# Kernel tuning notes

Hardware: AMD Instinct MI355X
Metric: run time of the kernel (lower is better)

The kernel has to match this reference:

```python
import jax, jax.numpy as jnp
import numpy as np

N_NODES = 20000


def _segment_softmax(alpha, dst, num_nodes):
    # numerically-stable softmax over edges grouped by destination node
    m = jax.ops.segment_max(alpha, dst, num_segments=num_nodes)
    m = jnp.where(jnp.isfinite(m), m, 0.0)
    a = jnp.exp(alpha - m[dst])
    denom = jax.ops.segment_sum(a, dst, num_segments=num_nodes)
    return a / denom[dst]


def mgcn_conv(x, src, dst, edge_type, basis, att, weight, root, bias, num_nodes):
    # x: [N, in], basis: [B, in, out], att: [R, B], weight: [R, out=in]
    x_i = x[dst]                                   # [E, in] target feats
    x_j = x[src]                                   # [E, in] source feats
    # per-edge attention logit: sum_d x_i[d] * w_r[d] * x_j[d]
    alpha = jnp.sum(x_i * weight[edge_type] * x_j, axis=1)   # [E]
    alpha = _segment_softmax(alpha, dst, num_nodes)          # [E]
    # basis-decomposed per-edge transform: x_j @ (att_r . basis)
    t = jnp.einsum('ei,bio->ebo', x_j, basis)                # [E, B, out]
    msg = jnp.einsum('ebo,eb->eo', t, att[edge_type])        # [E, out]
    msg = msg * alpha[:, None]
    out = jax.ops.segment_sum(msg, dst, num_segments=num_nodes)  # [N, out]
    return out + x @ root + bias


def setup_inputs() -> dict:
    key = jax.random.key(0)
    ks = jax.random.split(key, 16)
    E, D, R, B, N = 32768, 128, 474, 64, N_NODES
    s = 0.05
    return {
        'entity': jnp.arange(N, dtype=jnp.int64) if jax.config.jax_enable_x64 else jnp.arange(N, dtype=jnp.int32),
        'edge_index': jax.random.randint(ks[0], (2, E), 0, N, dtype=jnp.int32),
        'edge_type': jax.random.randint(ks[1], (E,), 0, R, dtype=jnp.int32),
        'emb_table': jax.random.normal(ks[2], (N, D), dtype=jnp.float32),
        'basis1': jax.random.normal(ks[3], (B, D, D), dtype=jnp.float32) * s,
        'att1': jax.random.normal(ks[4], (R, B), dtype=jnp.float32) * s,
        'weight1': jax.random.normal(ks[5], (R, D), dtype=jnp.float32) * s,
        'root1': jax.random.normal(ks[6], (D, D), dtype=jnp.float32) * s,
        'bias1': jnp.zeros((D,), dtype=jnp.float32),
        'basis2': jax.random.normal(ks[7], (B, D, D), dtype=jnp.float32) * s,
        'att2': jax.random.normal(ks[8], (R, B), dtype=jnp.float32) * s,
        'weight2': jax.random.normal(ks[9], (R, D), dtype=jnp.float32) * s,
        'root2': jax.random.normal(ks[10], (D, D), dtype=jnp.float32) * s,
        'bias2': jnp.zeros((D,), dtype=jnp.float32),
    }


def reference(entity, edge_index, edge_type, emb_table,
              basis1, att1, weight1, root1, bias1,
              basis2, att2, weight2, root2, bias2):
    src, dst = edge_index[0], edge_index[1]   # PyG: (source j, target i)
    x = emb_table[entity]                     # embedding lookup
    h = jax.nn.relu(mgcn_conv(x, src, dst, edge_type, basis1, att1,
                              weight1, root1, bias1, N_NODES))
    # dropout is identity at inference
    out = mgcn_conv(h, src, dst, edge_type, basis2, att2,
                    weight2, root2, bias2, N_NODES)
    return out
```

## Files before the change

### kernel.cpp

```cpp
#include <hip/hip_runtime.h>
#include <hip/hip_bf16.h>

#define N_NODES 20000
#define N_EDGES 32768
#define DIM 128
#define N_REL 474
#define N_BASIS 64
#define TILE_E 64
#define WSTRIDE 264
#define WMIX_BLKS 128
#define TR_BLKS 2
#define GATHER_BASE (WMIX_BLKS + TR_BLKS)
#define FIN_BLKS ((N_NODES + 63) / 64)
#define LELIST 1024

typedef __bf16 bf16x8 __attribute__((ext_vector_type(8)));
typedef float f32x4 __attribute__((ext_vector_type(4)));

__device__ __forceinline__ unsigned short f2b(float f) {
    unsigned u = __float_as_uint(f);
    unsigned r = (u + 0x7FFFu + ((u >> 16) & 1u)) >> 16;
    return (unsigned short)r;
}
__device__ __forceinline__ float b2f(unsigned short s) {
    return __uint_as_float(((unsigned)s) << 16);
}
__device__ __forceinline__ __bf16 u2b(unsigned short u) {
    union { unsigned short u; __bf16 b; } c; c.u = u; return c.b;
}
__device__ __forceinline__ float dot2bf(unsigned a, unsigned b, float wx, float wy) {
    return b2f((unsigned short)(a & 0xFFFFu)) * wx * b2f((unsigned short)(b & 0xFFFFu))
         + b2f((unsigned short)(a >> 16)) * wy * b2f((unsigned short)(b >> 16));
}

__global__ __launch_bounds__(256) void prep_kernel(const float4* __restrict__ emb,
                                                   const int* __restrict__ entity,
                                                   ushort4* __restrict__ xb4,
                                                   float4* __restrict__ zreg, int zcount4,
                                                   const float* __restrict__ att1,
                                                   const float* __restrict__ basis1,
                                                   unsigned short* __restrict__ W1,
                                                   const float* __restrict__ att2,
                                                   const float* __restrict__ basis2,
                                                   unsigned short* __restrict__ W2,
                                                   const float* __restrict__ root1,
                                                   unsigned short* __restrict__ rootT1,
                                                   const float* __restrict__ root2,
                                                   unsigned short* __restrict__ rootT2) {
    __shared__ __align__(16) unsigned short bt[64 * WSTRIDE];
    int t = threadIdx.x;
    if (blockIdx.x < WMIX_BLKS) {
        int wi = blockIdx.x;
        const float* att   = (wi >= 64) ? att2 : att1;
        const float* basis = (wi >= 64) ? basis2 : basis1;
        unsigned short* W  = (wi >= 64) ? W2 : W1;
        int io0 = (wi & 63) * 256;
#pragma unroll
        for (int p = 0; p < 16; p++) {
            int c = t + 256 * p;
            int k = c >> 6, of = c & 63;
            float4 v = *(const float4*)(basis + (size_t)k * (DIM * DIM) + io0 + of * 4);
            ushort4 s;
            s.x = f2b(v.x); s.y = f2b(v.y); s.z = f2b(v.z); s.w = f2b(v.w);
            int ofx = of ^ (((k >> 3) & 7) << 2);
            *(ushort4*)&bt[k * WSTRIDE + ofx * 4] = s;
        }
        __syncthreads();

        int w = t >> 6, l = t & 63, n = l & 15, q = l >> 4;
        bf16x8 bfr[2][4];
#pragma unroll
        for (int kb = 0; kb < 2; kb++) {
            int kbase = kb * 32 + q * 8;
            int sx = ((kb * 4 + q) & 7) << 4;
#pragma unroll
            for (int c = 0; c < 4; c++) {
                int ob = (w * 64 + c * 16 + n) ^ sx;
#pragma unroll
                for (int j = 0; j < 8; j++) bfr[kb][c][j] = u2b(bt[(kbase + j) * WSTRIDE + ob]);
            }
        }
#pragma unroll 1
        for (int rg = 0; rg < 8; rg++) {
            int r0 = rg * 64;
            f32x4 acc[4][4] = {};
#pragma unroll
            for (int kb = 0; kb < 2; kb++) {
                int kbase = kb * 32 + q * 8;
                bf16x8 a[4];
#pragma unroll
                for (int rt = 0; rt < 4; rt++) {
                    int rm = min(r0 + rt * 16 + n, N_REL - 1);
                    const float4* ap = (const float4*)(att + (size_t)rm * N_BASIS + kbase);
                    float4 u0 = ap[0], u1 = ap[1];
                    a[rt][0] = (__bf16)u0.x; a[rt][1] = (__bf16)u0.y;
                    a[rt][2] = (__bf16)u0.z; a[rt][3] = (__bf16)u0.w;
                    a[rt][4] = (__bf16)u1.x; a[rt][5] = (__bf16)u1.y;
                    a[rt][6] = (__bf16)u1.z; a[rt][7] = (__bf16)u1.w;
                }
#pragma unroll
                for (int c = 0; c < 4; c++) {
#pragma unroll
                    for (int rt = 0; rt < 4; rt++)
                        acc[rt][c] = __builtin_amdgcn_mfma_f32_16x16x32_bf16(a[rt], bfr[kb][c], acc[rt][c], 0, 0, 0);
                }
            }
#pragma unroll
            for (int rt = 0; rt < 4; rt++) {
#pragma unroll
                for (int c = 0; c < 4; c++) {
                    int col = io0 + w * 64 + c * 16 + n;
#pragma unroll
                    for (int g = 0; g < 4; g++) {
                        int r = r0 + rt * 16 + q * 4 + g;
                        if (r < N_REL) W[(size_t)r * (DIM * DIM) + col] = f2b(acc[rt][c][g]);
                    }
                }
            }
        }
    } else if (blockIdx.x < GATHER_BASE) {
        int wi2 = blockIdx.x - WMIX_BLKS;
        const float* rm = wi2 ? root2 : root1;
        unsigned short* rt_ = wi2 ? rootT2 : rootT1;
        unsigned short* sb16 = bt;
#pragma unroll
        for (int p = 0; p < 16; p++) {
            int idx = t + 256 * p;
            int k = idx >> 5, o4 = idx & 31;
            float4 v = ((const float4*)rm)[idx];
            ushort4 s;
            s.x = f2b(v.x); s.y = f2b(v.y); s.z = f2b(v.z); s.w = f2b(v.w);
            *(ushort4*)&sb16[k * 132 + o4 * 4] = s;
        }
        __syncthreads();
        int o = t >> 1, kh = (t & 1) * 64;
#pragma unroll
        for (int i = 0; i < 16; i++) {
            int k0 = kh + i * 4;
            ushort4 s;
            s.x = sb16[(k0 + 0) * 132 + o];
            s.y = sb16[(k0 + 1) * 132 + o];
            s.z = sb16[(k0 + 2) * 132 + o];
            s.w = sb16[(k0 + 3) * 132 + o];
            *(ushort4*)&rt_[o * DIM + k0] = s;
        }
    } else {
        int pb = blockIdx.x - GATHER_BASE;
        int gtid = pb * 256 + t;
        int gsz = 1024 * 256;
        int total4 = N_NODES * DIM / 4;
        for (int i = gtid; i < total4; i += gsz) {
            int n = i >> 5, rem = i & 31;
            float4 v = emb[(size_t)entity[n] * 32 + rem];
            ushort4 s;
            s.x = f2b(v.x); s.y = f2b(v.y); s.z = f2b(v.z); s.w = f2b(v.w);
            xb4[i] = s;
        }
        float4 z = make_float4(0.f, 0.f, 0.f, 0.f);
        for (int i = gtid; i < zcount4; i += gsz) zreg[i] = z;
    }
}

__global__ __launch_bounds__(256) void msg_kernel(const unsigned short* __restrict__ xb,
                                                  const unsigned short* __restrict__ W,
                                                  const float* __restrict__ wlog,
                                                  const int* __restrict__ src,
                                                  const int* __restrict__ dst,
                                                  const int* __restrict__ etype,
                                                  float* __restrict__ den,
                                                  float* __restrict__ accm) {
    int r = blockIdx.x;
    const unsigned short* Wr = W + (size_t)r * (DIM * DIM);

    __shared__ __align__(16) unsigned short wt[128 * 136];
    __shared__ __align__(16) unsigned short xjf[8192];
    __shared__ __align__(16) float wf[DIM];
    __shared__ float scf[TILE_E];
    __shared__ int sdd[TILE_E];
    __shared__ int ssrc[TILE_E];
    __shared__ int elist[LELIST];
    __shared__ int lcnt;

    int t = threadIdx.x;
    if (t == 0) lcnt = 0;
#pragma unroll
    for (int p = 0; p < 8; p++) {
        int c = t + 256 * p;
        int k = c >> 4, oct = c & 15;
        int4 v = *(const int4*)(Wr + k * DIM + oct * 8);
        int oct2 = oct ^ (((k >> 3) & 7) << 1);
        *(int4*)&wt[k * 136 + oct2 * 8] = v;
    }
    if (t < 32) ((float4*)wf)[t] = ((const float4*)(wlog + (size_t)r * DIM))[t];
    __syncthreads();

    int lane = t & 63;
    for (int it = 0; it < N_EDGES / 1024; it++) {
        int idx = it * 256 + t;
        int4 ev = ((const int4*)etype)[idx];
#pragma unroll
        for (int j = 0; j < 4; j++) {
            int etj = (j == 0) ? ev.x : (j == 1) ? ev.y : (j == 2) ? ev.z : ev.w;
            bool m = (etj == r);
            unsigned long long bal = __ballot(m);
            int tot = __popcll(bal);
            if (tot) {
                int base = 0;
                if (lane == 0) base = atomicAdd(&lcnt, tot);
                base = __shfl(base, 0, 64);
                if (m) {
                    int pre = __popcll(bal & ((1ull << lane) - 1ull));
                    int p_ = base + pre;
                    if (p_ < LELIST) elist[p_] = idx * 4 + j;
                }
            }
        }
    }
    __syncthreads();
    int cnt = min(lcnt, LELIST);
    if (cnt == 0) return;

    int w = t >> 6, l = t & 63, n = l & 15, q = l >> 4;
    int el4 = t >> 2, l4 = t & 3;

    for (int t0 = 0; t0 < cnt; t0 += TILE_E) {
        int nE = min(TILE_E, cnt - t0);
        if (t < TILE_E) {
            if (t < nE) {
                int e = elist[t0 + t];
                ssrc[t] = src[e];
                sdd[t]  = dst[e];
            } else { ssrc[t] = 0; sdd[t] = 0; }
        }
        __syncthreads();

        {
            int s_ = ssrc[el4], d_ = sdd[el4];
            const int4* xj = (const int4*)(xb + (size_t)s_ * DIM) + l4 * 4;
            const int4* xi = (const int4*)(xb + (size_t)d_ * DIM) + l4 * 4;
            const float4* wv = (const float4*)&wf[l4 * 32];
            float v = 0.f;
#pragma unroll
            for (int u = 0; u < 4; u++) {
                int4 a = xj[u]; int4 b = xi[u];
                float4 w0 = wv[u * 2], w1 = wv[u * 2 + 1];
                v += dot2bf((unsigned)a.x, (unsigned)b.x, w0.x, w0.y)
                   + dot2bf((unsigned)a.y, (unsigned)b.y, w0.z, w0.w)
                   + dot2bf((unsigned)a.z, (unsigned)b.z, w1.x, w1.y)
                   + dot2bf((unsigned)a.w, (unsigned)b.w, w1.z, w1.w);
            }
            v += __shfl_xor(v, 1, 64);
            v += __shfl_xor(v, 2, 64);
            if (l4 == 0) {
                if (el4 < nE) {
                    float a = expf(v);
                    scf[el4] = a;
                    atomicAdd(&den[d_], a);
                } else scf[el4] = 0.f;
            }
        }

#pragma unroll
        for (int p = 0; p < 4; p++) {
            int c = t + 256 * p;
            int g = c >> 6;
            int rt = g >> 2, kb = g & 3;
            int q2 = (c >> 4) & 3, m = c & 15;
            int e = rt * 16 + m;
            int oct = kb * 4 + q2;
            int4 v = make_int4(0, 0, 0, 0);
            if (e < nE) v = *(const int4*)(xb + (size_t)ssrc[e] * DIM + oct * 8);
            *(int4*)&xjf[c * 8] = v;
        }
        __syncthreads();

        f32x4 acc[2][4] = {};
#pragma unroll
        for (int kb = 0; kb < 4; kb++) {
            bf16x8 a[4];
#pragma unroll
            for (int rt = 0; rt < 4; rt++) a[rt] = *(const bf16x8*)&xjf[((rt * 4 + kb) * 64 + l) * 8];
            int kbase = kb * 32 + q * 8;
            int sx = ((kb * 4 + q) & 7) << 4;
#pragma unroll
            for (int c = 0; c < 2; c++) {
                int ob = ((w * 2 + c) * 16 + n) ^ sx;
                bf16x8 b;
#pragma unroll
                for (int j = 0; j < 8; j++) b[j] = u2b(wt[(kbase + j) * 136 + ob]);
#pragma unroll
                for (int rt = 0; rt < 4; rt++)
                    acc[c][rt] = __builtin_amdgcn_mfma_f32_16x16x32_bf16(a[rt], b, acc[c][rt], 0, 0, 0);
            }
        }
#pragma unroll
        for (int c = 0; c < 2; c++) {
            int col = (w * 2 + c) * 16 + n;
#pragma unroll
            for (int rt = 0; rt < 4; rt++) {
#pragma unroll
                for (int rg = 0; rg < 4; rg++) {
                    int e = rt * 16 + q * 4 + rg;
                    if (e < nE)
                        atomicAdd(&accm[(size_t)sdd[e] * DIM + col], scf[e] * acc[c][rt][rg]);
                }
            }
        }
        __syncthreads();
    }
}

__global__ __launch_bounds__(256) void fin_kernel(const unsigned short* __restrict__ xb,
                                                  const unsigned short* __restrict__ rootT,
                                                  const float* __restrict__ bias,
                                                  const float* __restrict__ accm,
                                                  const float* __restrict__ den,
                                                  float* __restrict__ outf,
                                                  unsigned short* __restrict__ outb) {
    __shared__ __align__(16) unsigned short xrf[8192];
    int t = threadIdx.x;
    int n0 = blockIdx.x * 64;
#pragma unroll
    for (int p = 0; p < 4; p++) {
        int c = t + 256 * p;
        int g = c >> 6;
        int rt = g >> 2, kb = g & 3;
        int q = (c >> 4) & 3, m = c & 15;
        int row = n0 + rt * 16 + m;
        int oct = kb * 4 + q;
        int4 v = make_int4(0, 0, 0, 0);
        if (row < N_NODES) v = *(const int4*)(xb + (size_t)row * DIM + oct * 8);
        *(int4*)&xrf[c * 8] = v;
    }
    __syncthreads();

    int w_ = t >> 6, l = t & 63, n = l & 15, q = l >> 4;
    f32x4 acc[2][4] = {};
#pragma unroll
    for (int kb = 0; kb < 4; kb++) {
        bf16x8 a[4];
#pragma unroll
        for (int rt = 0; rt < 4; rt++) a[rt] = *(const bf16x8*)&xrf[((rt * 4 + kb) * 64 + l) * 8];
        int kbase = kb * 32 + q * 8;
#pragma unroll
        for (int c = 0; c < 2; c++) {
            int col = (w_ * 2 + c) * 16 + n;
            bf16x8 b = *(const bf16x8*)(rootT + (size_t)col * DIM + kbase);
#pragma unroll
            for (int rt = 0; rt < 4; rt++)
                acc[c][rt] = __builtin_amdgcn_mfma_f32_16x16x32_bf16(a[rt], b, acc[c][rt], 0, 0, 0);
        }
    }
#pragma unroll
    for (int c = 0; c < 2; c++) {
        int col = (w_ * 2 + c) * 16 + n;
        float bo = bias[col];
#pragma unroll
        for (int rt = 0; rt < 4; rt++) {
#pragma unroll
            for (int rg = 0; rg < 4; rg++) {
                int row = n0 + rt * 16 + q * 4 + rg;
                if (row < N_NODES) {
                    float dv = den[row];
                    float mv = accm[(size_t)row * DIM + col];
                    float val = acc[c][rt][rg] + bo + (dv > 0.f ? mv / dv : 0.f);
                    if (outb) outb[(size_t)row * DIM + col] = f2b(fmaxf(val, 0.f));
                    else      outf[(size_t)row * DIM + col] = val;
                }
            }
        }
    }
}

extern "C" void kernel_launch(void* const* d_in, const int* in_sizes, int n_in,
                              void* d_out, int out_size, void* d_ws, size_t ws_size,
                              hipStream_t stream) {
    const int N = N_NODES, E = N_EDGES, R = N_REL;

    const int* entity = (const int*)d_in[0];
    const int* eidx   = (const int*)d_in[1];
    const int* src    = eidx;
    const int* dst    = eidx + E;
    const int* etype  = (const int*)d_in[2];
    const float* emb  = (const float*)d_in[3];
    const float* basis1 = (const float*)d_in[4];
    const float* att1   = (const float*)d_in[5];
    const float* w1     = (const float*)d_in[6];
    const float* root1  = (const float*)d_in[7];
    const float* bias1  = (const float*)d_in[8];
    const float* basis2 = (const float*)d_in[9];
    const float* att2   = (const float*)d_in[10];
    const float* w2     = (const float*)d_in[11];
    const float* root2  = (const float*)d_in[12];
    const float* bias2  = (const float*)d_in[13];
    float* out = (float*)d_out;

    size_t off = 0;
    auto alloc = [&](size_t bytes) -> void* {
        void* p = (char*)d_ws + off;
        off += (bytes + 255) & ~(size_t)255;
        return p;
    };
    unsigned short* W1 = (unsigned short*)alloc((size_t)R * DIM * DIM * 2);
    unsigned short* W2 = (unsigned short*)alloc((size_t)R * DIM * DIM * 2);
    unsigned short* xb = (unsigned short*)alloc((size_t)N * DIM * 2);
    unsigned short* hb = (unsigned short*)alloc((size_t)N * DIM * 2);
    float* zreg   = (float*)alloc(((size_t)2 * N + (size_t)2 * N * DIM) * 4);
    float* den1   = zreg;
    float* den2   = zreg + N;
    float* accm1  = zreg + 2 * N;
    float* accm2  = zreg + 2 * N + (size_t)N * DIM;
    unsigned short* rootT1 = (unsigned short*)alloc((size_t)DIM * DIM * 2);
    unsigned short* rootT2 = (unsigned short*)alloc((size_t)DIM * DIM * 2);

    int zcount4 = (2 * N + 2 * N * DIM) / 4;

    prep_kernel<<<GATHER_BASE + 1024, 256, 0, stream>>>(
        (const float4*)emb, entity, (ushort4*)xb, (float4*)zreg, zcount4,
        att1, basis1, W1, att2, basis2, W2, root1, rootT1, root2, rootT2);

    msg_kernel<<<N_REL, 256, 0, stream>>>(xb, W1, w1, src, dst, etype, den1, accm1);
    fin_kernel<<<FIN_BLKS, 256, 0, stream>>>(xb, rootT1, bias1, accm1, den1, nullptr, hb);

    msg_kernel<<<N_REL, 256, 0, stream>>>(hb, W2, w2, src, dst, etype, den2, accm2);
    fin_kernel<<<FIN_BLKS, 256, 0, stream>>>(hb, rootT2, bias2, accm2, den2, out, nullptr);
}
```

Baseline: 227.9 us.

## Split relation blocks in half, fold root GEMM into prep/msg, add merge kernel

Each relation now gets two message blocks, each scanning half of the edge types, which doubles the grid to spread work across more CUs. The root (x @ root) GEMM moves out of the finalize kernel: for layer 1 it runs inside prep blocks, and for layer 2 as extra blocks in the message kernel. A lightweight vectorized merge kernel then combines root, message and denominator. The W mix output is staged through LDS so global stores are 16-byte vectorized. In exchange it writes and reads extra fp32 racc buffers and adds redundant W tile loads per relation half.

New measurement: 215.3 us. 5.5% less time.

```diff
diff --git a/kernel.cpp b/kernel.cpp
--- a/kernel.cpp
+++ b/kernel.cpp
@@ -8,11 +8,17 @@
 #define N_BASIS 64
 #define TILE_E 64
 #define WSTRIDE 264
+#define LELIST 1024
+
 #define WMIX_BLKS 128
-#define TR_BLKS 2
-#define GATHER_BASE (WMIX_BLKS + TR_BLKS)
-#define FIN_BLKS ((N_NODES + 63) / 64)
-#define LELIST 1024
+#define ROOTT_BLK 1
+#define RG1_BASE (WMIX_BLKS + ROOTT_BLK)
+#define RG1_BLKS ((N_NODES + 63) / 64)
+#define GATHER_BASE (RG1_BASE + RG1_BLKS)
+#define PREP_GRID 1024
+
+#define MSG_REL_BLKS (2 * N_REL)
+#define MERGE_GRID 1024
 
 typedef __bf16 bf16x8 __attribute__((ext_vector_type(8)));
 typedef float f32x4 __attribute__((ext_vector_type(4)));
@@ -27,6 +33,14 @@
 }
 __device__ __forceinline__ __bf16 u2b(unsigned short u) {
     union { unsigned short u; __bf16 b; } c; c.u = u; return c.b;
+}
+__device__ __forceinline__ int4 pack8(float4 a0, float4 a1) {
+    int4 v;
+    v.x = (int)((unsigned)f2b(a0.x) | ((unsigned)f2b(a0.y) << 16));
+    v.y = (int)((unsigned)f2b(a0.z) | ((unsigned)f2b(a0.w) << 16));
+    v.z = (int)((unsigned)f2b(a1.x) | ((unsigned)f2b(a1.y) << 16));
+    v.w = (int)((unsigned)f2b(a1.z) | ((unsigned)f2b(a1.w) << 16));
+    return v;
 }
 __device__ __forceinline__ float dot2bf(unsigned a, unsigned b, float wx, float wy) {
     return b2f((unsigned short)(a & 0xFFFFu)) * wx * b2f((unsigned short)(b & 0xFFFFu))
@@ -44,7 +58,7 @@
                                                    const float* __restrict__ basis2,
                                                    unsigned short* __restrict__ W2,
                                                    const float* __restrict__ root1,
-                                                   unsigned short* __restrict__ rootT1,
+                                                   float* __restrict__ racc1,
                                                    const float* __restrict__ root2,
                                                    unsigned short* __restrict__ rootT2) {
     __shared__ __align__(16) unsigned short bt[64 * WSTRIDE];
@@ -80,6 +94,9 @@
                 for (int j = 0; j < 8; j++) bfr[kb][c][j] = u2b(bt[(kbase + j) * WSTRIDE + ob]);
             }
         }
+        __syncthreads();
+
+        int srow = t >> 2, sseg = t & 3;
 #pragma unroll 1
         for (int rg = 0; rg < 8; rg++) {
             int r0 = rg * 64;
@@ -109,25 +126,32 @@
             for (int rt = 0; rt < 4; rt++) {
 #pragma unroll
                 for (int c = 0; c < 4; c++) {
-                    int col = io0 + w * 64 + c * 16 + n;
-#pragma unroll
-                    for (int g = 0; g < 4; g++) {
-                        int r = r0 + rt * 16 + q * 4 + g;
-                        if (r < N_REL) W[(size_t)r * (DIM * DIM) + col] = f2b(acc[rt][c][g]);
-                    }
-                }
-            }
-        }
-    } else if (blockIdx.x < GATHER_BASE) {
-        int wi2 = blockIdx.x - WMIX_BLKS;
-        const float* rm = wi2 ? root2 : root1;
-        unsigned short* rt_ = wi2 ? rootT2 : rootT1;
+#pragma unroll
+                    for (int g = 0; g < 4; g++)
+                        bt[(rt * 16 + q * 4 + g) * WSTRIDE + w * 64 + c * 16 + n] = f2b(acc[rt][c][g]);
+                }
+            }
+            __syncthreads();
+            int rr = r0 + srow;
+            if (rr < N_REL) {
+                const int4* sp = (const int4*)&bt[srow * WSTRIDE];
+                unsigned short* wp = W + (size_t)rr * (DIM * DIM) + io0;
+#pragma unroll
+                for (int ii = 0; ii < 8; ii++) {
+                    int i = (ii + sseg * 2) & 7;
+                    int4 v = sp[sseg * 8 + i];
+                    *(int4*)(wp + sseg * 64 + i * 8) = v;
+                }
+            }
+            __syncthreads();
+        }
+    } else if (blockIdx.x < RG1_BASE) {
         unsigned short* sb16 = bt;
 #pragma unroll
         for (int p = 0; p < 16; p++) {
             int idx = t + 256 * p;
             int k = idx >> 5, o4 = idx & 31;
-            float4 v = ((const float4*)rm)[idx];
+            float4 v = ((const float4*)root2)[idx];
             ushort4 s;
             s.x = f2b(v.x); s.y = f2b(v.y); s.z = f2b(v.z); s.w = f2b(v.w);
             *(ushort4*)&sb16[k * 132 + o4 * 4] = s;
@@ -142,12 +166,64 @@
             s.y = sb16[(k0 + 1) * 132 + o];
             s.z = sb16[(k0 + 2) * 132 + o];
             s.w = sb16[(k0 + 3) * 132 + o];
-            *(ushort4*)&rt_[o * DIM + k0] = s;
+            *(ushort4*)&rootT2[o * DIM + k0] = s;
+        }
+    } else if (blockIdx.x < GATHER_BASE) {
+        int n0 = (blockIdx.x - RG1_BASE) * 64;
+        unsigned short* xrf = bt;
+#pragma unroll
+        for (int p = 0; p < 4; p++) {
+            int c = t + 256 * p;
+            int g = c >> 6;
+            int rt = g >> 2, kb = g & 3;
+            int q2 = (c >> 4) & 3, m = c & 15;
+            int row = n0 + rt * 16 + m;
+            int oct = kb * 4 + q2;
+            int4 v = make_int4(0, 0, 0, 0);
+            if (row < N_NODES) {
+                const float4* sp = emb + (size_t)entity[row] * 32 + oct * 2;
+                v = pack8(sp[0], sp[1]);
+            }
+            *(int4*)&xrf[c * 8] = v;
+        }
+        __syncthreads();
+
+        int w_ = t >> 6, l = t & 63, n = l & 15, q = l >> 4;
+        f32x4 acc[2][4] = {};
+#pragma unroll
+        for (int kb = 0; kb < 4; kb++) {
+            bf16x8 a[4];
+#pragma unroll
+            for (int rt = 0; rt < 4; rt++) a[rt] = *(const bf16x8*)&xrf[((rt * 4 + kb) * 64 + l) * 8];
+            int kbase = kb * 32 + q * 8;
+#pragma unroll
+            for (int c = 0; c < 2; c++) {
+                int col = (w_ * 2 + c) * 16 + n;
+                bf16x8 b;
+#pragma unroll
+                for (int j = 0; j < 8; j++) b[j] = (__bf16)root1[(kbase + j) * DIM + col];
+#pragma unroll
+                for (int rt = 0; rt < 4; rt++)
+                    acc[c][rt] = __builtin_amdgcn_mfma_f32_16x16x32_bf16(a[rt], b, acc[c][rt], 0, 0, 0);
+            }
+        }
+#pragma unroll
+        for (int c = 0; c < 2; c++) {
+            int col = (w_ * 2 + c) * 16 + n;
+#pragma unroll
+            for (int rt = 0; rt < 4; rt++) {
+#pragma unroll
+                for (int rg = 0; rg < 4; rg++) {
+                    int row = n0 + rt * 16 + q * 4 + rg;
+                    if (row < N_NODES)
+                        racc1[(size_t)row * DIM + col] = acc[c][rt][rg];
+                }
+            }
         }
     } else {
         int pb = blockIdx.x - GATHER_BASE;
         int gtid = pb * 256 + t;
-        int gsz = 1024 * 256;
+        int gsz = (PREP_GRID - GATHER_BASE) * 256;
         int total4 = N_NODES * DIM / 4;
         for (int i = gtid; i < total4; i += gsz) {
             int n = i >> 5, rem = i & 31;
@@ -168,10 +244,9 @@
                                                   const int* __restrict__ dst,
                                                   const int* __restrict__ etype,
                                                   float* __restrict__ den,
-                                                  float* __restrict__ accm) {
-    int r = blockIdx.x;
-    const unsigned short* Wr = W + (size_t)r * (DIM * DIM);
-
+                                                  float* __restrict__ accm,
+                                                  const unsigned short* __restrict__ rootT,
+                                                  float* __restrict__ racc) {
     __shared__ __align__(16) unsigned short wt[128 * 136];
     __shared__ __align__(16) unsigned short xjf[8192];
     __shared__ __align__(16) float wf[DIM];
@@ -182,192 +257,213 @@
     __shared__ int lcnt;
 
     int t = threadIdx.x;
-    if (t == 0) lcnt = 0;
-#pragma unroll
-    for (int p = 0; p < 8; p++) {
-        int c = t + 256 * p;
-        int k = c >> 4, oct = c & 15;
-        int4 v = *(const int4*)(Wr + k * DIM + oct * 8);
-        int oct2 = oct ^ (((k >> 3) & 7) << 1);
-        *(int4*)&wt[k * 136 + oct2 * 8] = v;
-    }
-    if (t < 32) ((float4*)wf)[t] = ((const float4*)(wlog + (size_t)r * DIM))[t];
-    __syncthreads();
-
-    int lane = t & 63;
-    for (int it = 0; it < N_EDGES / 1024; it++) {
-        int idx = it * 256 + t;
-        int4 ev = ((const int4*)etype)[idx];
-#pragma unroll
-        for (int j = 0; j < 4; j++) {
-            int etj = (j == 0) ? ev.x : (j == 1) ? ev.y : (j == 2) ? ev.z : ev.w;
-            bool m = (etj == r);
-            unsigned long long bal = __ballot(m);
-            int tot = __popcll(bal);
-            if (tot) {
-                int base = 0;
-                if (lane == 0) base = atomicAdd(&lcnt, tot);
-                base = __shfl(base, 0, 64);
-                if (m) {
-                    int pre = __popcll(bal & ((1ull << lane) - 1ull));
-                    int p_ = base + pre;
-                    if (p_ < LELIST) elist[p_] = idx * 4 + j;
-                }
-            }
-        }
-    }
-    __syncthreads();
-    int cnt = min(lcnt, LELIST);
-    if (cnt == 0) return;
-
-    int w = t >> 6, l = t & 63, n = l & 15, q = l >> 4;
-    int el4 = t >> 2, l4 = t & 3;
-
-    for (int t0 = 0; t0 < cnt; t0 += TILE_E) {
-        int nE = min(TILE_E, cnt - t0);
-        if (t < TILE_E) {
-            if (t < nE) {
-                int e = elist[t0 + t];
-                ssrc[t] = src[e];
-                sdd[t]  = dst[e];
-            } else { ssrc[t] = 0; sdd[t] = 0; }
-        }
-        __syncthreads();
-
-        {
-            int s_ = ssrc[el4], d_ = sdd[el4];
-            const int4* xj = (const int4*)(xb + (size_t)s_ * DIM) + l4 * 4;
-            const int4* xi = (const int4*)(xb + (size_t)d_ * DIM) + l4 * 4;
-            const float4* wv = (const float4*)&wf[l4 * 32];
-            float v = 0.f;
-#pragma unroll
-            for (int u = 0; u < 4; u++) {
-                int4 a = xj[u]; int4 b = xi[u];
-                float4 w0 = wv[u * 2], w1 = wv[u * 2 + 1];
-                v += dot2bf((unsigned)a.x, (unsigned)b.x, w0.x, w0.y)
-                   + dot2bf((unsigned)a.y, (unsigned)b.y, w0.z, w0.w)
-                   + dot2bf((unsigned)a.z, (unsigned)b.z, w1.x, w1.y)
-                   + dot2bf((unsigned)a.w, (unsigned)b.w, w1.z, w1.w);
-            }
-            v += __shfl_xor(v, 1, 64);
-            v += __shfl_xor(v, 2, 64);
-            if (l4 == 0) {
-                if (el4 < nE) {
-                    float a = expf(v);
-                    scf[el4] = a;
-                    atomicAdd(&den[d_], a);
-                } else scf[el4] = 0.f;
-            }
-        }
-
+    if ((int)blockIdx.x < MSG_REL_BLKS) {
+        int r = blockIdx.x >> 1, half = blockIdx.x & 1;
+        const unsigned short* Wr = W + (size_t)r * (DIM * DIM);
+        if (t == 0) lcnt = 0;
+#pragma unroll
+        for (int p = 0; p < 8; p++) {
+            int c = t + 256 * p;
+            int k = c >> 4, oct = c & 15;
+            int4 v = *(const int4*)(Wr + k * DIM + oct * 8);
+            int oct2 = oct ^ (((k >> 3) & 7) << 1);
+            *(int4*)&wt[k * 136 + oct2 * 8] = v;
+        }
+        if (t < 32) ((float4*)wf)[t] = ((const float4*)(wlog + (size_t)r * DIM))[t];
+        __syncthreads();
+
+        int lane = t & 63;
+        for (int it = half * 16; it < half * 16 + 16; it++) {
+            int idx = it * 256 + t;
+            int4 ev = ((const int4*)etype)[idx];
+#pragma unroll
+            for (int j = 0; j < 4; j++) {
+                int etj = (j == 0) ? ev.x : (j == 1) ? ev.y : (j == 2) ? ev.z : ev.w;
+                bool m = (etj == r);
+                unsigned long long bal = __ballot(m);
+                int tot = __popcll(bal);
+                if (tot) {
+                    int base = 0;
+                    if (lane == 0) base = atomicAdd(&lcnt, tot);
+                    base = __shfl(base, 0, 64);
+                    if (m) {
+                        int pre = __popcll(bal & ((1ull << lane) - 1ull));
+                        int p_ = base + pre;
+                        if (p_ < LELIST) elist[p_] = idx * 4 + j;
+                    }
+                }
+            }
+        }
+        __syncthreads();
+        int cnt = min(lcnt, LELIST);
+        if (cnt == 0) return;
+
+        int w = t >> 6, l = t & 63, n = l & 15, q = l >> 4;
+        int el4 = t >> 2, l4 = t & 3;
+
+        for (int t0 = 0; t0 < cnt; t0 += TILE_E) {
+            int nE = min(TILE_E, cnt - t0);
+            if (t < TILE_E) {
+                if (t < nE) {
+                    int e = elist[t0 + t];
+                    ssrc[t] = src[e];
+                    sdd[t]  = dst[e];
+                } else { ssrc[t] = 0; sdd[t] = 0; }
+            }
+            __syncthreads();
+
+            {
+                int s_ = ssrc[el4], d_ = sdd[el4];
+                const int4* xj = (const int4*)(xb + (size_t)s_ * DIM) + l4 * 4;
+                const int4* xi = (const int4*)(xb + (size_t)d_ * DIM) + l4 * 4;
+                const float4* wv = (const float4*)&wf[l4 * 32];
+                float v = 0.f;
+#pragma unroll
+                for (int u = 0; u < 4; u++) {
+                    int4 a = xj[u]; int4 bb = xi[u];
+                    float4 w0 = wv[u * 2], w1 = wv[u * 2 + 1];
+                    v += dot2bf((unsigned)a.x, (unsigned)bb.x, w0.x, w0.y)
+                       + dot2bf((unsigned)a.y, (unsigned)bb.y, w0.z, w0.w)
+                       + dot2bf((unsigned)a.z, (unsigned)bb.z, w1.x, w1.y)
+                       + dot2bf((unsigned)a.w, (unsigned)bb.w, w1.z, w1.w);
+                }
+                v += __shfl_xor(v, 1, 64);
+                v += __shfl_xor(v, 2, 64);
+                if (l4 == 0) {
+                    if (el4 < nE) {
+                        float a = expf(v);
+                        scf[el4] = a;
+                        atomicAdd(&den[d_], a);
+                    } else scf[el4] = 0.f;
+                }
+            }
+
+#pragma unroll
+            for (int p = 0; p < 4; p++) {
+                int c = t + 256 * p;
+                int g = c >> 6;
+                int rt = g >> 2, kb = g & 3;
+                int q2 = (c >> 4) & 3, m = c & 15;
+                int e = rt * 16 + m;
+                int oct = kb * 4 + q2;
+                int4 v = make_int4(0, 0, 0, 0);
+                if (e < nE) v = *(const int4*)(xb + (size_t)ssrc[e] * DIM + oct * 8);
+                *(int4*)&xjf[c * 8] = v;
+            }
+            __syncthreads();
+
+            f32x4 acc[2][4] = {};
+#pragma unroll
+            for (int kb = 0; kb < 4; kb++) {
+                bf16x8 a[4];
+#pragma unroll
+                for (int rt = 0; rt < 4; rt++) a[rt] = *(const bf16x8*)&xjf[((rt * 4 + kb) * 64 + l) * 8];
+                int kbase = kb * 32 + q * 8;
+                int sx = ((kb * 4 + q) & 7) << 4;
+#pragma unroll
+                for (int c = 0; c < 2; c++) {
+                    int ob = ((w * 2 + c) * 16 + n) ^ sx;
+                    bf16x8 bb;
+#pragma unroll
+                    for (int j = 0; j < 8; j++) bb[j] = u2b(wt[(kbase + j) * 136 + ob]);
+#pragma unroll
+                    for (int rt = 0; rt < 4; rt++)
+                        acc[c][rt] = __builtin_amdgcn_mfma_f32_16x16x32_bf16(a[rt], bb, acc[c][rt], 0, 0, 0);
+                }
+            }
+#pragma unroll
+            for (int c = 0; c < 2; c++) {
+                int col = (w * 2 + c) * 16 + n;
+#pragma unroll
+                for (int rt = 0; rt < 4; rt++) {
+#pragma unroll
+                    for (int rg = 0; rg < 4; rg++) {
+                        int e = rt * 16 + q * 4 + rg;
+                        if (e < nE)
+                            atomicAdd(&accm[(size_t)sdd[e] * DIM + col], scf[e] * acc[c][rt][rg]);
+                    }
+                }
+            }
+            __syncthreads();
+        }
+    } else {
+        int n0 = ((int)blockIdx.x - MSG_REL_BLKS) * 64;
+        unsigned short* xrf = wt;
 #pragma unroll
         for (int p = 0; p < 4; p++) {
             int c = t + 256 * p;
             int g = c >> 6;
             int rt = g >> 2, kb = g & 3;
             int q2 = (c >> 4) & 3, m = c & 15;
-            int e = rt * 16 + m;
+            int row = n0 + rt * 16 + m;
             int oct = kb * 4 + q2;
             int4 v = make_int4(0, 0, 0, 0);
-            if (e < nE) v = *(const int4*)(xb + (size_t)ssrc[e] * DIM + oct * 8);
-            *(int4*)&xjf[c * 8] = v;
-        }
-        __syncthreads();
-
+            if (row < N_NODES) v = *(const int4*)(xb + (size_t)row * DIM + oct * 8);
+            *(int4*)&xrf[c * 8] = v;
+        }
+        __syncthreads();
+
+        int w_ = t >> 6, l = t & 63, n = l & 15, q = l >> 4;
         f32x4 acc[2][4] = {};
 #pragma unroll
         for (int kb = 0; kb < 4; kb++) {
             bf16x8 a[4];
 #pragma unroll
-            for (int rt = 0; rt < 4; rt++) a[rt] = *(const bf16x8*)&xjf[((rt * 4 + kb) * 64 + l) * 8];
+            for (int rt = 0; rt < 4; rt++) a[rt] = *(const bf16x8*)&xrf[((rt * 4 + kb) * 64 + l) * 8];
             int kbase = kb * 32 + q * 8;
-            int sx = ((kb * 4 + q) & 7) << 4;
 #pragma unroll
             for (int c = 0; c < 2; c++) {
-                int ob = ((w * 2 + c) * 16 + n) ^ sx;
-                bf16x8 b;
-#pragma unroll
-                for (int j = 0; j < 8; j++) b[j] = u2b(wt[(kbase + j) * 136 + ob]);
+                int col = (w_ * 2 + c) * 16 + n;
+                bf16x8 bb = *(const bf16x8*)(rootT + (size_t)col * DIM + kbase);
 #pragma unroll
                 for (int rt = 0; rt < 4; rt++)
-                    acc[c][rt] = __builtin_amdgcn_mfma_f32_16x16x32_bf16(a[rt], b, acc[c][rt], 0, 0, 0);
-            }
-        }
-#pragma unroll
-        for (int c = 0; c < 2; c++) {
-            int col = (w * 2 + c) * 16 + n;
-#pragma unroll
-            for (int rt = 0; rt < 4; rt++) {
-#pragma unroll
-                for (int rg = 0; rg < 4; rg++) {
-                    int e = rt * 16 + q * 4 + rg;
-                    if (e < nE)
-                        atomicAdd(&accm[(size_t)sdd[e] * DIM + col], scf[e] * acc[c][rt][rg]);
-                }
-            }
-        }
-        __syncthreads();
-    }
-}
-
-__global__ __launch_bounds__(256) void fin_kernel(const unsigned short* __restrict__ xb,
-                                                  const unsigned short* __restrict__ rootT,
-                                                  const float* __restrict__ bias,
-                                                  const float* __restrict__ accm,
-                                                  const float* __restrict__ den,
-                                                  float* __restrict__ outf,
-                                                  unsigned short* __restrict__ outb) {
-    __shared__ __align__(16) unsigned short xrf[8192];
-    int t = threadIdx.x;
-    int n0 = blockIdx.x * 64;
-#pragma unroll
-    for (int p = 0; p < 4; p++) {
-        int c = t + 256 * p;
-        int g = c >> 6;
-        int rt = g >> 2, kb = g & 3;
-        int q = (c >> 4) & 3, m = c & 15;
-        int row = n0 + rt * 16 + m;
-        int oct = kb * 4 + q;
-        int4 v = make_int4(0, 0, 0, 0);
-        if (row < N_NODES) v = *(const int4*)(xb + (size_t)row * DIM + oct * 8);
-        *(int4*)&xrf[c * 8] = v;
-    }
-    __syncthreads();
-
-    int w_ = t >> 6, l = t & 63, n = l & 15, q = l >> 4;
-    f32x4 acc[2][4] = {};
-#pragma unroll
-    for (int kb = 0; kb < 4; kb++) {
-        bf16x8 a[4];
-#pragma unroll
-        for (int rt = 0; rt < 4; rt++) a[rt] = *(const bf16x8*)&xrf[((rt * 4 + kb) * 64 + l) * 8];
-        int kbase = kb * 32 + q * 8;
+                    acc[c][rt] = __builtin_amdgcn_mfma_f32_16x16x32_bf16(a[rt], bb, acc[c][rt], 0, 0, 0);
+            }
+        }
 #pragma unroll
         for (int c = 0; c < 2; c++) {
             int col = (w_ * 2 + c) * 16 + n;
-            bf16x8 b = *(const bf16x8*)(rootT + (size_t)col * DIM + kbase);
-#pragma unroll
-            for (int rt = 0; rt < 4; rt++)
-                acc[c][rt] = __builtin_amdgcn_mfma_f32_16x16x32_bf16(a[rt], b, acc[c][rt], 0, 0, 0);
+#pragma unroll
+            for (int rt = 0; rt < 4; rt++) {
+#pragma unroll
+                for (int rg = 0; rg < 4; rg++) {
+                    int row = n0 + rt * 16 + q * 4 + rg;
+                    if (row < N_NODES)
+                        racc[(size_t)row * DIM + col] = acc[c][rt][rg];
+                }
+            }
         }
     }
-#pragma unroll
-    for (int c = 0; c < 2; c++) {
-        int col = (w_ * 2 + c) * 16 + n;
-        float bo = bias[col];
-#pragma unroll
-        for (int rt = 0; rt < 4; rt++) {
-#pragma unroll
-            for (int rg = 0; rg < 4; rg++) {
-                int row = n0 + rt * 16 + q * 4 + rg;
-                if (row < N_NODES) {
-                    float dv = den[row];
-                    float mv = accm[(size_t)row * DIM + col];
-                    float val = acc[c][rt][rg] + bo + (dv > 0.f ? mv / dv : 0.f);
-                    if (outb) outb[(size_t)row * DIM + col] = f2b(fmaxf(val, 0.f));
-                    else      outf[(size_t)row * DIM + col] = val;
-                }
-            }
+}
+
+__global__ __launch_bounds__(256) void merge_kernel(const float4* __restrict__ racc,
+                                                    const float4* __restrict__ accm,
+                                                    const float* __restrict__ den,
+                                                    const float* __restrict__ bias,
+                                                    float4* __restrict__ outf,
+                                                    ushort4* __restrict__ outb) {
+    int gtid = blockIdx.x * 256 + threadIdx.x;
+    const int tot4 = N_NODES * (DIM / 4);
+    for (int i = gtid; i < tot4; i += (int)gridDim.x * 256) {
+        int row = i >> 5;
+        int c0 = (i & 31) * 4;
+        float4 rv = racc[i];
+        float4 mv = accm[i];
+        float4 bo = *(const float4*)&bias[c0];
+        float dv = den[row];
+        float inv = dv > 0.f ? 1.0f / dv : 0.f;
+        float4 v;
+        v.x = rv.x + bo.x + mv.x * inv;
+        v.y = rv.y + bo.y + mv.y * inv;
+        v.z = rv.z + bo.z + mv.z * inv;
+        v.w = rv.w + bo.w + mv.w * inv;
+        if (outb) {
+            ushort4 s;
+            s.x = f2b(fmaxf(v.x, 0.f)); s.y = f2b(fmaxf(v.y, 0.f));
+            s.z = f2b(fmaxf(v.z, 0.f)); s.w = f2b(fmaxf(v.w, 0.f));
+            outb[i] = s;
+        } else {
+            outf[i] = v;
         }
     }
 }
@@ -405,23 +501,28 @@
     unsigned short* W2 = (unsigned short*)alloc((size_t)R * DIM * DIM * 2);
     unsigned short* xb = (unsigned short*)alloc((size_t)N * DIM * 2);
     unsigned short* hb = (unsigned short*)alloc((size_t)N * DIM * 2);
+    float* racc1  = (float*)alloc((size_t)N * DIM * 4);
+    float* racc2  = (float*)alloc((size_t)N * DIM * 4);
     float* zreg   = (float*)alloc(((size_t)2 * N + (size_t)2 * N * DIM) * 4);
     float* den1   = zreg;
     float* den2   = zreg + N;
     float* accm1  = zreg + 2 * N;
     float* accm2  = zreg + 2 * N + (size_t)N * DIM;
-    unsigned short* rootT1 = (unsigned short*)alloc((size_t)DIM * DIM * 2);
     unsigned short* rootT2 = (unsigned short*)alloc((size_t)DIM * DIM * 2);
 
     int zcount4 = (2 * N + 2 * N * DIM) / 4;
 
-    prep_kernel<<<GATHER_BASE + 1024, 256, 0, stream>>>(
+    prep_kernel<<<PREP_GRID, 256, 0, stream>>>(
         (const float4*)emb, entity, (ushort4*)xb, (float4*)zreg, zcount4,
-        att1, basis1, W1, att2, basis2, W2, root1, rootT1, root2, rootT2);
-
-    msg_kernel<<<N_REL, 256, 0, stream>>>(xb, W1, w1, src, dst, etype, den1, accm1);
-    fin_kernel<<<FIN_BLKS, 256, 0, stream>>>(xb, rootT1, bias1, accm1, den1, nullptr, hb);
-
-    msg_kernel<<<N_REL, 256, 0, stream>>>(hb, W2, w2, src, dst, etype, den2, accm2);
-    fin_kernel<<<FIN_BLKS, 256, 0, stream>>>(hb, rootT2, bias2, accm2, den2, out, nullptr);
-}
+        att1, basis1, W1, att2, basis2, W2, root1, racc1, root2, rootT2);
+
+    msg_kernel<<<MSG_REL_BLKS, 256, 0, stream>>>(xb, W1, w1, src, dst, etype,
+                                                 den1, accm1, nullptr, nullptr);
+    merge_kernel<<<MERGE_GRID, 256, 0, stream>>>((const float4*)racc1, (const float4*)accm1,
+                                                 den1, bias1, nullptr, (ushort4*)hb);
+
+    msg_kernel<<<MSG_REL_BLKS + RG1_BLKS, 256, 0, stream>>>(hb, W2, w2, src, dst, etype,
+                                                            den2, accm2, rootT2, racc2);
+    merge_kernel<<<MERGE_GRID, 256, 0, stream>>>((const float4*)racc2, (const float4*)accm2,
+                                                 den2, bias2, (float4*)out, nullptr);
+}
```
